# Performance work log

Measured on AMD Instinct MI355X. Metric: run time of the kernel, lower is better.

## Reference

```python
import jax, jax.numpy as jnp
import numpy as np

D_MODEL = 512
N_HEADS = 8
D_K = D_MODEL // N_HEADS
D_DTW = 21


def setup_inputs() -> dict:
    key = jax.random.key(0)
    ks = jax.random.split(key, 16)
    bs, S = 16, 512
    def lin(k, fan_in, shape):
        return jax.random.uniform(k, shape, jnp.float32, -1.0, 1.0) / np.sqrt(fan_in)
    return {
        "Q": jax.random.normal(ks[0], (bs, S, D_MODEL), jnp.float32),
        "K": jax.random.normal(ks[1], (bs, S, D_MODEL), jnp.float32),
        "V": jax.random.normal(ks[2], (bs, S, D_MODEL), jnp.float32),
        "G": jax.random.normal(ks[3], (bs, S, D_MODEL), jnp.float32),
        "dtw_cost": jax.random.uniform(ks[4], (bs, D_DTW, S, S), jnp.float32),
        "Wq": lin(ks[5], D_MODEL, (D_MODEL, D_MODEL)), "bq": lin(ks[6], D_MODEL, (D_MODEL,)),
        "Wk": lin(ks[7], D_MODEL, (D_MODEL, D_MODEL)), "bk": lin(ks[8], D_MODEL, (D_MODEL,)),
        "Wv": lin(ks[9], D_MODEL, (D_MODEL, D_MODEL)), "bv": lin(ks[10], D_MODEL, (D_MODEL,)),
        "Wd": lin(ks[11], D_DTW, (N_HEADS, D_DTW)), "bd": lin(ks[12], D_DTW, (N_HEADS,)),
        "Wo": lin(ks[13], D_MODEL, (D_MODEL, D_MODEL)), "bo": lin(ks[14], D_MODEL, (D_MODEL,)),
    }


def reference(Q, K, V, G, dtw_cost, Wq, bq, Wk, bk, Wv, bv, Wd, bd, Wo, bo):
    bs, S, _ = Q.shape
    # QKV projections, split into heads: [bs, H, S, dk]
    def proj(x, W, b):
        y = x @ W.T + b
        return y.reshape(bs, S, N_HEADS, D_K).transpose(0, 2, 1, 3)
    q = proj(Q, Wq, bq)
    k = proj(K, Wk, bk)
    v = proj(V, Wv, bv)
    # scaled dot-product scores [bs, H, S, S]
    scores = jnp.einsum("bhqd,bhkd->bhqk", q, k) / np.sqrt(D_K).astype(np.float32)
    # DTW-cost bias: linear over the cost-channel dim (21 -> H), added per head
    bias = jnp.einsum("bcqk,hc->bhqk", dtw_cost, Wd) + bd[None, :, None, None]
    attn = jax.nn.softmax(scores + bias, axis=-1)
    out = jnp.einsum("bhqk,bhkd->bhqd", attn, v)  # [bs, H, S, dk]
    concat = out.transpose(0, 2, 1, 3).reshape(bs, S, D_MODEL)
    output = concat @ Wo.T + bo
    return (output, attn)
```

## Files before the change

kernel.cpp:

```cpp
#include <hip/hip_runtime.h>
#include <hip/hip_bf16.h>
#include <cstddef>
#include <cstdint>

#define BS   16
#define SLEN 512
#define DM   512
#define NH   8
#define DK   64
#define DC   21

typedef __attribute__((ext_vector_type(8))) short short8;
typedef __attribute__((ext_vector_type(4))) float f32x4;

__device__ inline unsigned pack_bf16(float a, float b) {
    unsigned ua = __builtin_bit_cast(unsigned, a);
    unsigned ub = __builtin_bit_cast(unsigned, b);
    ua = (ua + 0x7fffu + ((ua >> 16) & 1u)) >> 16;
    ub = (ub + 0x7fffu + ((ub >> 16) & 1u)) >> 16;
    return ua | (ub << 16);
}

__device__ inline unsigned cvt2(float a, float b) { return pack_bf16(a, b); }

__global__ __launch_bounds__(256) void gemm_bf16(
    const float* __restrict__ X, const float* __restrict__ W,
    const float* __restrict__ bias, void* __restrict__ outv, int mode)
{
    __shared__ alignas(16) ushort Atile[64 * 64];
    __shared__ alignas(16) ushort Btile[128 * 64];

    const int tid = threadIdx.x;
    const int wave = tid >> 6, lane = tid & 63;
    const int lq = lane & 15, lg = lane >> 4;
    const int wr = wave >> 1, wc = wave & 1;
    const int m0 = blockIdx.x * 64;
    const int n0 = blockIdx.y * 128;

    f32x4 acc[2][4];
#pragma unroll
    for (int i = 0; i < 2; ++i)
#pragma unroll
        for (int j = 0; j < 4; ++j) acc[i][j] = (f32x4){0.f, 0.f, 0.f, 0.f};

    float4 pa[2][2], pb[4][2];

#define LOAD_A(K0)                                                          \
    _Pragma("unroll")                                                       \
    for (int i = 0; i < 2; ++i) {                                           \
        const int P = tid + 256 * i;                                        \
        const int row = P >> 3, cp = P & 7;                                 \
        const float4* s = (const float4*)&X[(size_t)(m0 + row) * 512 + (K0) + cp * 8]; \
        pa[i][0] = s[0]; pa[i][1] = s[1];                                   \
    }
#define LOAD_B(K0)                                                          \
    _Pragma("unroll")                                                       \
    for (int i = 0; i < 4; ++i) {                                           \
        const int P = tid + 256 * i;                                        \
        const int row = P >> 3, cp = P & 7;                                 \
        const float4* s = (const float4*)&W[(size_t)(n0 + row) * 512 + (K0) + cp * 8]; \
        pb[i][0] = s[0]; pb[i][1] = s[1];                                   \
    }

    LOAD_A(0)
    LOAD_B(0)

    for (int it = 0; it < 8; ++it) {
        __syncthreads();
#pragma unroll
        for (int i = 0; i < 2; ++i) {
            const int P = tid + 256 * i;
            const int row = P >> 3, cp = P & 7;
            uint4 w;
            w.x = cvt2(pa[i][0].x, pa[i][0].y);
            w.y = cvt2(pa[i][0].z, pa[i][0].w);
            w.z = cvt2(pa[i][1].x, pa[i][1].y);
            w.w = cvt2(pa[i][1].z, pa[i][1].w);
            *(uint4*)((char*)Atile + row * 128 + 16 * (cp ^ (row & 7))) = w;
        }
#pragma unroll
        for (int i = 0; i < 4; ++i) {
            const int P = tid + 256 * i;
            const int row = P >> 3, cp = P & 7;
            uint4 w;
            w.x = cvt2(pb[i][0].x, pb[i][0].y);
            w.y = cvt2(pb[i][0].z, pb[i][0].w);
            w.z = cvt2(pb[i][1].x, pb[i][1].y);
            w.w = cvt2(pb[i][1].z, pb[i][1].w);
            *(uint4*)((char*)Btile + row * 128 + 16 * (cp ^ (row & 7))) = w;
        }
        __syncthreads();

        if (it < 7) {
            const int kn = (it + 1) * 64;
            LOAD_A(kn)
            LOAD_B(kn)
        }

        short8 af[2][2], bfr[4][2];
#pragma unroll
        for (int mi = 0; mi < 2; ++mi)
#pragma unroll
            for (int kh = 0; kh < 2; ++kh) {
                const int row = wr * 32 + mi * 16 + lq;
                af[mi][kh] = *(const short8*)((const char*)Atile + row * 128 +
                                              16 * ((kh * 4 + lg) ^ (row & 7)));
            }
#pragma unroll
        for (int ni = 0; ni < 4; ++ni)
#pragma unroll
            for (int kh = 0; kh < 2; ++kh) {
                const int row = wc * 64 + ni * 16 + lq;
                bfr[ni][kh] = *(const short8*)((const char*)Btile + row * 128 +
                                               16 * ((kh * 4 + lg) ^ (row & 7)));
            }
#pragma unroll
        for (int kh = 0; kh < 2; ++kh)
#pragma unroll
            for (int mi = 0; mi < 2; ++mi)
#pragma unroll
                for (int ni = 0; ni < 4; ++ni)
                    acc[mi][ni] = __builtin_amdgcn_mfma_f32_16x16x32_bf16(
                        af[mi][kh], bfr[ni][kh], acc[mi][ni], 0, 0, 0);
    }
#undef LOAD_A
#undef LOAD_B

    if (mode == 0) {
        float* out = (float*)outv;
#pragma unroll
        for (int mi = 0; mi < 2; ++mi) {
            const int mb = m0 + wr * 32 + mi * 16 + lg * 4;
#pragma unroll
            for (int ni = 0; ni < 4; ++ni) {
                const int n = n0 + wc * 64 + ni * 16 + lq;
                const float bb = bias[n];
#pragma unroll
                for (int r = 0; r < 4; ++r)
                    out[(size_t)(mb + r) * 512 + n] = acc[mi][ni][r] + bb;
            }
        }
    } else if (mode == 1) {
        ushort* out = (ushort*)outv;
#pragma unroll
        for (int mi = 0; mi < 2; ++mi) {
            const int mb = m0 + wr * 32 + mi * 16 + lg * 4;
#pragma unroll
            for (int ni = 0; ni < 4; ++ni) {
                const int n = n0 + wc * 64 + ni * 16 + lq;
                const int h = n >> 6, d = n & 63;
                const float bb = bias[n];
#pragma unroll
                for (int r = 0; r < 4; ++r) {
                    const int m = mb + r;
                    const int bidx = m >> 9, s = m & 511;
                    const float v = acc[mi][ni][r] + bb;
                    out[((size_t)(bidx * NH + h) * SLEN + s) * DK + d] =
                        (ushort)(pack_bf16(v, 0.f) & 0xffffu);
                }
            }
        }
    } else {
        ushort* out = (ushort*)outv;
#pragma unroll
        for (int mi = 0; mi < 2; ++mi) {
            const int mb = m0 + wr * 32 + mi * 16 + lg * 4;
            const int bidx = mb >> 9, s0 = mb & 511;
#pragma unroll
            for (int ni = 0; ni < 4; ++ni) {
                const int n = n0 + wc * 64 + ni * 16 + lq;
                const int h = n >> 6, d = n & 63;
                const float bb = bias[n];
                uint2 pk;
                pk.x = cvt2(acc[mi][ni][0] + bb, acc[mi][ni][1] + bb);
                pk.y = cvt2(acc[mi][ni][2] + bb, acc[mi][ni][3] + bb);
                *(uint2*)&out[((size_t)(bidx * NH + h) * DK + d) * SLEN + s0] = pk;
            }
        }
    }
}

__global__ __launch_bounds__(512) void bias_kernel(
    const float* __restrict__ dtw, const float* __restrict__ Wd,
    const float* __restrict__ bd, float* __restrict__ bias_out)
{
    __shared__ float wdl[NH * DC];
    __shared__ float bdl[NH];
    const int k = threadIdx.x;
    const int q = blockIdx.x;
    const int b = blockIdx.y;
    if (k < NH * DC) wdl[k] = Wd[k];
    if (k < NH) bdl[k] = bd[k];
    __syncthreads();

    float acc[NH];
#pragma unroll
    for (int h = 0; h < NH; ++h) acc[h] = bdl[h];

    const float* p = dtw + ((size_t)b * DC * SLEN + q) * SLEN + k;
#pragma unroll
    for (int c = 0; c < DC; ++c) {
        const float x = p[(size_t)c * SLEN * SLEN];
#pragma unroll
        for (int h = 0; h < NH; ++h) acc[h] += x * wdl[h * DC + c];
    }
#pragma unroll
    for (int h = 0; h < NH; ++h)
        bias_out[((size_t)(b * NH + h) * SLEN + q) * SLEN + k] = acc[h];
}

__global__ __launch_bounds__(256, 2) void attn_mfma(
    const ushort* __restrict__ qb, const ushort* __restrict__ kb,
    const ushort* __restrict__ vt, float* __restrict__ attn,
    float* __restrict__ concat)
{
    __shared__ ushort P_lds[4][16][512];

    const int tid = threadIdx.x;
    const int wave = tid >> 6;
    const int lane = tid & 63;
    const int lq = lane & 15;
    const int lg = lane >> 4;
    const int qt = blockIdx.x;
    const int h = blockIdx.y, b = blockIdx.z;
    const int bh = b * NH + h;
    const int q0 = qt * 64 + wave * 16;

    const ushort* qptr = qb + ((size_t)bh * SLEN + q0) * DK;
    const ushort* kptr = kb + (size_t)bh * SLEN * DK;
    const ushort* vptr = vt + (size_t)bh * DK * SLEN;
    float* attn_b = attn + ((size_t)bh * SLEN + q0) * SLEN;

    const short8 qf0 = *(const short8*)&qptr[(size_t)lq * DK + lg * 8];
    const short8 qf1 = *(const short8*)&qptr[(size_t)lq * DK + lg * 8 + 32];

    const float* bias_row = attn_b + (size_t)lq * SLEN;

    f32x4 sc[32];
#pragma unroll
    for (int kt = 0; kt < 32; ++kt) {
        const short8 a0 = *(const short8*)&kptr[(size_t)(kt * 16 + lq) * DK + lg * 8];
        const short8 a1 = *(const short8*)&kptr[(size_t)(kt * 16 + lq) * DK + lg * 8 + 32];
        f32x4 c = {0.f, 0.f, 0.f, 0.f};
        c = __builtin_amdgcn_mfma_f32_16x16x32_bf16(a0, qf0, c, 0, 0, 0);
        c = __builtin_amdgcn_mfma_f32_16x16x32_bf16(a1, qf1, c, 0, 0, 0);
        const f32x4 bias4 = *(const f32x4*)&bias_row[kt * 16 + lg * 4];
        sc[kt] = c * 0.125f + bias4;
    }

    float m = -1e30f;
#pragma unroll
    for (int kt = 0; kt < 32; ++kt)
        m = fmaxf(m, fmaxf(fmaxf(sc[kt][0], sc[kt][1]), fmaxf(sc[kt][2], sc[kt][3])));
    m = fmaxf(m, __shfl_xor(m, 16));
    m = fmaxf(m, __shfl_xor(m, 32));

    float sum = 0.f;
#pragma unroll
    for (int kt = 0; kt < 32; ++kt) {
        f32x4 e;
        e[0] = __expf(sc[kt][0] - m);
        e[1] = __expf(sc[kt][1] - m);
        e[2] = __expf(sc[kt][2] - m);
        e[3] = __expf(sc[kt][3] - m);
        sum += (e[0] + e[1]) + (e[2] + e[3]);
        sc[kt] = e;
    }
    sum += __shfl_xor(sum, 16);
    sum += __shfl_xor(sum, 32);
    const float inv = 1.0f / sum;

    char* pbase = (char*)&P_lds[wave][0][0];
    const unsigned swz = (unsigned)((lq & 7) << 4);
#pragma unroll
    for (int kt = 0; kt < 32; ++kt) {
        const f32x4 e = sc[kt];
        f32x4 a4 = e * inv;
        *(f32x4*)&attn_b[(size_t)lq * SLEN + kt * 16 + lg * 4] = a4;
        uint2 pk;
        pk.x = pack_bf16(e[0], e[1]);
        pk.y = pack_bf16(e[2], e[3]);
        const unsigned byte = (unsigned)(lq * 1024 + kt * 32 + lg * 8) ^ swz;
        *(uint2*)(pbase + byte) = pk;
    }
    asm volatile("s_waitcnt lgkmcnt(0)" ::: "memory");
    __builtin_amdgcn_sched_barrier(0);

    f32x4 oacc[4] = {{0.f,0.f,0.f,0.f},{0.f,0.f,0.f,0.f},{0.f,0.f,0.f,0.f},{0.f,0.f,0.f,0.f}};
#pragma unroll
    for (int c = 0; c < 16; ++c) {
        const unsigned byteA = (unsigned)(lq * 1024 + c * 64 + lg * 16) ^ swz;
        const short8 pa = *(const short8*)(pbase + byteA);
#pragma unroll
        for (int dt = 0; dt < 4; ++dt) {
            const short8 vb8 = *(const short8*)&vptr[(size_t)(dt * 16 + lq) * SLEN + c * 32 + lg * 8];
            oacc[dt] = __builtin_amdgcn_mfma_f32_16x16x32_bf16(pa, vb8, oacc[dt], 0, 0, 0);
        }
    }

    float* cbase = concat + ((size_t)(b * SLEN + q0)) * DM + h * 64;
#pragma unroll
    for (int r = 0; r < 4; ++r) {
        const float iv = __shfl(inv, lg * 4 + r);
#pragma unroll
        for (int dt = 0; dt < 4; ++dt) {
            cbase[(size_t)(lg * 4 + r) * DM + dt * 16 + lq] = oacc[dt][r] * iv;
        }
    }
}

extern "C" void kernel_launch(void* const* d_in, const int* in_sizes, int n_in,
                              void* d_out, int out_size, void* d_ws, size_t ws_size,
                              hipStream_t stream)
{
    const float* Q   = (const float*)d_in[0];
    const float* K   = (const float*)d_in[1];
    const float* V   = (const float*)d_in[2];
    const float* dtw = (const float*)d_in[4];
    const float* Wq  = (const float*)d_in[5];
    const float* bq  = (const float*)d_in[6];
    const float* Wk  = (const float*)d_in[7];
    const float* bk  = (const float*)d_in[8];
    const float* Wv  = (const float*)d_in[9];
    const float* bv  = (const float*)d_in[10];
    const float* Wd  = (const float*)d_in[11];
    const float* bd  = (const float*)d_in[12];
    const float* Wo  = (const float*)d_in[13];
    const float* bo  = (const float*)d_in[14];

    float* out  = (float*)d_out;
    float* attn = out + (size_t)BS * SLEN * DM;

    const size_t PHS = (size_t)BS * NH * SLEN * DK;
    ushort* qb = (ushort*)d_ws;
    ushort* kb = qb + PHS;
    ushort* vt = kb + PHS;
    float*  cb = (float*)(vt + PHS);

    const dim3 gemm_grid(128, 4);

    gemm_bf16<<<gemm_grid, 256, 0, stream>>>(Q, Wq, bq, qb, 1);
    gemm_bf16<<<gemm_grid, 256, 0, stream>>>(K, Wk, bk, kb, 1);
    gemm_bf16<<<gemm_grid, 256, 0, stream>>>(V, Wv, bv, vt, 2);

    bias_kernel<<<dim3(SLEN, BS), 512, 0, stream>>>(dtw, Wd, bd, attn);

    attn_mfma<<<dim3(SLEN / 64, NH, BS), 256, 0, stream>>>(qb, kb, vt, attn, cb);

    gemm_bf16<<<gemm_grid, 256, 0, stream>>>(cb, Wo, bo, out, 0);
}
```

Baseline: 269.5 us.

## Store DTW bias as fp16 in attn buffer, bf16 concat, swizzled attention grid

The bias kernel now writes the DTW bias as fp16 into the first half of each 16-row chunk of the attn output buffer, rather than as fp32. This halves the bias write and re-read traffic, since each attention wave reads its bias before overwriting those rows with fp32 probabilities. The attention output is stored as bf16 and read directly by a templated output GEMM, which skips the fp32 read and convert step. Other changes: the attention grid is remapped to a 1D swizzled order, and s_setprio is raised around the MFMA sections. The cost is lower bias precision (fp16) and reliance on the in-place buffer aliasing.

```diff
diff --git a/kernel.cpp b/kernel.cpp
--- a/kernel.cpp
+++ b/kernel.cpp
@@ -12,6 +12,7 @@
 
 typedef __attribute__((ext_vector_type(8))) short short8;
 typedef __attribute__((ext_vector_type(4))) float f32x4;
+typedef __attribute__((ext_vector_type(4))) _Float16 h16x4;
 
 __device__ inline unsigned pack_bf16(float a, float b) {
     unsigned ua = __builtin_bit_cast(unsigned, a);
@@ -20,15 +21,23 @@
     ub = (ub + 0x7fffu + ((ub >> 16) & 1u)) >> 16;
     return ua | (ub << 16);
 }
-
 __device__ inline unsigned cvt2(float a, float b) { return pack_bf16(a, b); }
-
+__device__ inline ushort bf16_1(float a) { return (ushort)(pack_bf16(a, 0.f) & 0xffffu); }
+
+__device__ __host__ inline size_t bias_chunk_base(int bh, int q16) {
+    return 2 * (((size_t)bh * SLEN + (size_t)q16) * SLEN);
+}
+
+template<int MODE>
 __global__ __launch_bounds__(256) void gemm_bf16(
-    const float* __restrict__ X, const float* __restrict__ W,
-    const float* __restrict__ bias, void* __restrict__ outv, int mode)
+    const void* __restrict__ Xv, const float* __restrict__ W,
+    const float* __restrict__ bias, void* __restrict__ outv)
 {
     __shared__ alignas(16) ushort Atile[64 * 64];
     __shared__ alignas(16) ushort Btile[128 * 64];
+
+    const float*  Xf = (const float*)Xv;
+    const ushort* Xb = (const ushort*)Xv;
 
     const int tid = threadIdx.x;
     const int wave = tid >> 6, lane = tid & 63;
@@ -44,22 +53,32 @@
         for (int j = 0; j < 4; ++j) acc[i][j] = (f32x4){0.f, 0.f, 0.f, 0.f};
 
     float4 pa[2][2], pb[4][2];
-
-#define LOAD_A(K0)                                                          \
-    _Pragma("unroll")                                                       \
-    for (int i = 0; i < 2; ++i) {                                           \
-        const int P = tid + 256 * i;                                        \
-        const int row = P >> 3, cp = P & 7;                                 \
-        const float4* s = (const float4*)&X[(size_t)(m0 + row) * 512 + (K0) + cp * 8]; \
-        pa[i][0] = s[0]; pa[i][1] = s[1];                                   \
-    }
-#define LOAD_B(K0)                                                          \
-    _Pragma("unroll")                                                       \
-    for (int i = 0; i < 4; ++i) {                                           \
-        const int P = tid + 256 * i;                                        \
-        const int row = P >> 3, cp = P & 7;                                 \
+    uint4  qa[2];
+
+#define LOAD_A(K0)                                                              \
+    if (MODE == 3) {                                                            \
+        _Pragma("unroll")                                                       \
+        for (int i = 0; i < 2; ++i) {                                           \
+            const int P = tid + 256 * i;                                        \
+            const int row = P >> 3, sl = P & 7;                                 \
+            qa[i] = *(const uint4*)&Xb[(size_t)(m0 + row) * 512 + (K0) + sl * 8]; \
+        }                                                                       \
+    } else {                                                                    \
+        _Pragma("unroll")                                                       \
+        for (int i = 0; i < 2; ++i) {                                           \
+            const int P = tid + 256 * i;                                        \
+            const int row = P >> 3, cp = P & 7;                                 \
+            const float4* s = (const float4*)&Xf[(size_t)(m0 + row) * 512 + (K0) + cp * 8]; \
+            pa[i][0] = s[0]; pa[i][1] = s[1];                                   \
+        }                                                                       \
+    }
+#define LOAD_B(K0)                                                              \
+    _Pragma("unroll")                                                           \
+    for (int i = 0; i < 4; ++i) {                                               \
+        const int P = tid + 256 * i;                                            \
+        const int row = P >> 3, cp = P & 7;                                     \
         const float4* s = (const float4*)&W[(size_t)(n0 + row) * 512 + (K0) + cp * 8]; \
-        pb[i][0] = s[0]; pb[i][1] = s[1];                                   \
+        pb[i][0] = s[0]; pb[i][1] = s[1];                                       \
     }
 
     LOAD_A(0)
@@ -67,16 +86,25 @@
 
     for (int it = 0; it < 8; ++it) {
         __syncthreads();
-#pragma unroll
-        for (int i = 0; i < 2; ++i) {
-            const int P = tid + 256 * i;
-            const int row = P >> 3, cp = P & 7;
-            uint4 w;
-            w.x = cvt2(pa[i][0].x, pa[i][0].y);
-            w.y = cvt2(pa[i][0].z, pa[i][0].w);
-            w.z = cvt2(pa[i][1].x, pa[i][1].y);
-            w.w = cvt2(pa[i][1].z, pa[i][1].w);
-            *(uint4*)((char*)Atile + row * 128 + 16 * (cp ^ (row & 7))) = w;
+        if (MODE == 3) {
+#pragma unroll
+            for (int i = 0; i < 2; ++i) {
+                const int P = tid + 256 * i;
+                const int row = P >> 3, sl = P & 7;
+                *(uint4*)((char*)Atile + row * 128 + 16 * (sl ^ (row & 7))) = qa[i];
+            }
+        } else {
+#pragma unroll
+            for (int i = 0; i < 2; ++i) {
+                const int P = tid + 256 * i;
+                const int row = P >> 3, cp = P & 7;
+                uint4 w;
+                w.x = cvt2(pa[i][0].x, pa[i][0].y);
+                w.y = cvt2(pa[i][0].z, pa[i][0].w);
+                w.z = cvt2(pa[i][1].x, pa[i][1].y);
+                w.w = cvt2(pa[i][1].z, pa[i][1].w);
+                *(uint4*)((char*)Atile + row * 128 + 16 * (cp ^ (row & 7))) = w;
+            }
         }
 #pragma unroll
         for (int i = 0; i < 4; ++i) {
@@ -114,6 +142,7 @@
                 bfr[ni][kh] = *(const short8*)((const char*)Btile + row * 128 +
                                                16 * ((kh * 4 + lg) ^ (row & 7)));
             }
+        __builtin_amdgcn_s_setprio(1);
 #pragma unroll
         for (int kh = 0; kh < 2; ++kh)
 #pragma unroll
@@ -122,11 +151,12 @@
                 for (int ni = 0; ni < 4; ++ni)
                     acc[mi][ni] = __builtin_amdgcn_mfma_f32_16x16x32_bf16(
                         af[mi][kh], bfr[ni][kh], acc[mi][ni], 0, 0, 0);
+        __builtin_amdgcn_s_setprio(0);
     }
 #undef LOAD_A
 #undef LOAD_B
 
-    if (mode == 0) {
+    if (MODE == 3) {
         float* out = (float*)outv;
 #pragma unroll
         for (int mi = 0; mi < 2; ++mi) {
@@ -140,7 +170,7 @@
                     out[(size_t)(mb + r) * 512 + n] = acc[mi][ni][r] + bb;
             }
         }
-    } else if (mode == 1) {
+    } else if (MODE == 1) {
         ushort* out = (ushort*)outv;
 #pragma unroll
         for (int mi = 0; mi < 2; ++mi) {
@@ -154,9 +184,8 @@
                 for (int r = 0; r < 4; ++r) {
                     const int m = mb + r;
                     const int bidx = m >> 9, s = m & 511;
-                    const float v = acc[mi][ni][r] + bb;
                     out[((size_t)(bidx * NH + h) * SLEN + s) * DK + d] =
-                        (ushort)(pack_bf16(v, 0.f) & 0xffffu);
+                        bf16_1(acc[mi][ni][r] + bb);
                 }
             }
         }
@@ -182,7 +211,7 @@
 
 __global__ __launch_bounds__(512) void bias_kernel(
     const float* __restrict__ dtw, const float* __restrict__ Wd,
-    const float* __restrict__ bd, float* __restrict__ bias_out)
+    const float* __restrict__ bd, _Float16* __restrict__ bias16)
 {
     __shared__ float wdl[NH * DC];
     __shared__ float bdl[NH];
@@ -204,15 +233,18 @@
 #pragma unroll
         for (int h = 0; h < NH; ++h) acc[h] += x * wdl[h * DC + c];
     }
-#pragma unroll
-    for (int h = 0; h < NH; ++h)
-        bias_out[((size_t)(b * NH + h) * SLEN + q) * SLEN + k] = acc[h];
+    const int q16 = q & ~15, ql = q & 15;
+#pragma unroll
+    for (int h = 0; h < NH; ++h) {
+        const size_t base = bias_chunk_base(b * NH + h, q16);
+        bias16[base + (size_t)ql * SLEN + k] = (_Float16)acc[h];
+    }
 }
 
 __global__ __launch_bounds__(256, 2) void attn_mfma(
     const ushort* __restrict__ qb, const ushort* __restrict__ kb,
     const ushort* __restrict__ vt, float* __restrict__ attn,
-    float* __restrict__ concat)
+    ushort* __restrict__ concat)
 {
     __shared__ ushort P_lds[4][16][512];
 
@@ -221,8 +253,11 @@
     const int lane = tid & 63;
     const int lq = lane & 15;
     const int lg = lane >> 4;
-    const int qt = blockIdx.x;
-    const int h = blockIdx.y, b = blockIdx.z;
+
+    const unsigned l = blockIdx.x;
+    const int g  = (int)((l & 7) + 8 * (l >> 6));
+    const int qt = (int)((l >> 3) & 7);
+    const int h = g & 7, b = g >> 3;
     const int bh = b * NH + h;
     const int q0 = qt * 64 + wave * 16;
 
@@ -230,11 +265,11 @@
     const ushort* kptr = kb + (size_t)bh * SLEN * DK;
     const ushort* vptr = vt + (size_t)bh * DK * SLEN;
     float* attn_b = attn + ((size_t)bh * SLEN + q0) * SLEN;
+    const _Float16* bias_row =
+        (const _Float16*)attn + bias_chunk_base(bh, q0) + (size_t)lq * SLEN;
 
     const short8 qf0 = *(const short8*)&qptr[(size_t)lq * DK + lg * 8];
     const short8 qf1 = *(const short8*)&qptr[(size_t)lq * DK + lg * 8 + 32];
-
-    const float* bias_row = attn_b + (size_t)lq * SLEN;
 
     f32x4 sc[32];
 #pragma unroll
@@ -242,9 +277,14 @@
         const short8 a0 = *(const short8*)&kptr[(size_t)(kt * 16 + lq) * DK + lg * 8];
         const short8 a1 = *(const short8*)&kptr[(size_t)(kt * 16 + lq) * DK + lg * 8 + 32];
         f32x4 c = {0.f, 0.f, 0.f, 0.f};
+        __builtin_amdgcn_s_setprio(1);
         c = __builtin_amdgcn_mfma_f32_16x16x32_bf16(a0, qf0, c, 0, 0, 0);
         c = __builtin_amdgcn_mfma_f32_16x16x32_bf16(a1, qf1, c, 0, 0, 0);
-        const f32x4 bias4 = *(const f32x4*)&bias_row[kt * 16 + lg * 4];
+        __builtin_amdgcn_s_setprio(0);
+        const h16x4 bh4 = *(const h16x4*)&bias_row[kt * 16 + lg * 4];
+        f32x4 bias4;
+        bias4[0] = (float)bh4[0]; bias4[1] = (float)bh4[1];
+        bias4[2] = (float)bh4[2]; bias4[3] = (float)bh4[3];
         sc[kt] = c * 0.125f + bias4;
     }
 
@@ -291,20 +331,22 @@
     for (int c = 0; c < 16; ++c) {
         const unsigned byteA = (unsigned)(lq * 1024 + c * 64 + lg * 16) ^ swz;
         const short8 pa = *(const short8*)(pbase + byteA);
+        __builtin_amdgcn_s_setprio(1);
 #pragma unroll
         for (int dt = 0; dt < 4; ++dt) {
             const short8 vb8 = *(const short8*)&vptr[(size_t)(dt * 16 + lq) * SLEN + c * 32 + lg * 8];
             oacc[dt] = __builtin_amdgcn_mfma_f32_16x16x32_bf16(pa, vb8, oacc[dt], 0, 0, 0);
         }
-    }
-
-    float* cbase = concat + ((size_t)(b * SLEN + q0)) * DM + h * 64;
+        __builtin_amdgcn_s_setprio(0);
+    }
+
+    ushort* cbase = concat + ((size_t)(b * SLEN + q0)) * DM + h * 64;
 #pragma unroll
     for (int r = 0; r < 4; ++r) {
         const float iv = __shfl(inv, lg * 4 + r);
 #pragma unroll
         for (int dt = 0; dt < 4; ++dt) {
-            cbase[(size_t)(lg * 4 + r) * DM + dt * 16 + lq] = oacc[dt][r] * iv;
+            cbase[(size_t)(lg * 4 + r) * DM + dt * 16 + lq] = bf16_1(oacc[dt][r] * iv);
         }
     }
 }
@@ -330,22 +372,23 @@
 
     float* out  = (float*)d_out;
     float* attn = out + (size_t)BS * SLEN * DM;
+    _Float16* bias16 = (_Float16*)attn;
 
     const size_t PHS = (size_t)BS * NH * SLEN * DK;
     ushort* qb = (ushort*)d_ws;
     ushort* kb = qb + PHS;
     ushort* vt = kb + PHS;
-    float*  cb = (float*)(vt + PHS);
+    ushort* cb = vt + PHS;
 
     const dim3 gemm_grid(128, 4);
 
-    gemm_bf16<<<gemm_grid, 256, 0, stream>>>(Q, Wq, bq, qb, 1);
-    gemm_bf16<<<gemm_grid, 256, 0, stream>>>(K, Wk, bk, kb, 1);
-    gemm_bf16<<<gemm_grid, 256, 0, stream>>>(V, Wv, bv, vt, 2);
-
-    bias_kernel<<<dim3(SLEN, BS), 512, 0, stream>>>(dtw, Wd, bd, attn);
-
-    attn_mfma<<<dim3(SLEN / 64, NH, BS), 256, 0, stream>>>(qb, kb, vt, attn, cb);
-
-    gemm_bf16<<<gemm_grid, 256, 0, stream>>>(cb, Wo, bo, out, 0);
-}
+    gemm_bf16<1><<<gemm_grid, 256, 0, stream>>>(Q, Wq, bq, qb);
+    gemm_bf16<1><<<gemm_grid, 256, 0, stream>>>(K, Wk, bk, kb);
+    gemm_bf16<2><<<gemm_grid, 256, 0, stream>>>(V, Wv, bv, vt);
+
+    bias_kernel<<<dim3(SLEN, BS), 512, 0, stream>>>(dtw, Wd, bd, bias16);
+
+    attn_mfma<<<dim3(1024), 256, 0, stream>>>(qb, kb, vt, attn, cb);
+
+    gemm_bf16<3><<<gemm_grid, 256, 0, stream>>>(cb, Wo, bo, out);
+}
```

Result: no change. 269.9 us (+0.2%).
